# Kernel optimization log

Measured on AMD Instinct MI355X. Metric: run time of the kernel, lower is better.

Reference implementation:

```python
import jax, jax.numpy as jnp
import numpy as np

N_NODES = 50000
N_EDGES = 2000000
H = 64            # hidden_channels
D_IN = 2 * H      # concat(src, dst)
NEG_SLOPE = 0.01  # torch F.leaky_relu default


def _mlp_params(key, scale=0.05):
    ks = jax.random.split(key, 8)
    dims = [(D_IN, H), (H, H), (H, H // 2), (H // 2, 1)]
    p = []
    for i, (din, dout) in enumerate(dims):
        p.append(jax.random.normal(ks[2 * i], (din, dout), jnp.float32) * scale)
        p.append(jax.random.normal(ks[2 * i + 1], (dout,), jnp.float32) * scale)
    return p


def setup_inputs() -> dict:
    key = jax.random.key(0)
    k1, k2, k3, ke, kw = jax.random.split(key, 5)
    x_src = jax.random.normal(k1, (N_NODES, H), jnp.float32)
    x_dst = jax.random.normal(k2, (N_NODES, H), jnp.float32)
    edge_label_index = jax.random.randint(k3, (2, N_EDGES), 0, N_NODES, jnp.int64)
    e = _mlp_params(ke)
    w = _mlp_params(kw)
    inp = {"x_src": x_src, "x_dst": x_dst, "edge_label_index": edge_label_index}
    for i in range(4):
        inp[f"ew{i+1}"] = e[2 * i]; inp[f"eb{i+1}"] = e[2 * i + 1]
        inp[f"ww{i+1}"] = w[2 * i]; inp[f"wb{i+1}"] = w[2 * i + 1]
    return inp


def _mlp(x, w1, b1, w2, b2, w3, b3, w4, b4):
    lrelu = lambda z: jax.nn.leaky_relu(z, NEG_SLOPE)
    x = lrelu(x @ w1 + b1)
    x = lrelu(x @ w2 + b2)
    x = lrelu(x @ w3 + b3)
    return x @ w4 + b4


def reference(x_src, x_dst, edge_label_index,
              ew1, eb1, ww1, wb1, ew2, eb2, ww2, wb2,
              ew3, eb3, ww3, wb3, ew4, eb4, ww4, wb4):
    # gather node features by edge endpoints, concat -> [E, 2H]
    combined = jnp.concatenate(
        [x_src[edge_label_index[0]], x_dst[edge_label_index[1]]], axis=-1)
    link_exists = _mlp(combined, ew1, eb1, ew2, eb2, ew3, eb3, ew4, eb4)
    link_weight = _mlp(combined, ww1, wb1, ww2, wb2, ww3, wb3, ww4, wb4)
    return link_exists, link_weight
```

## Files before the change

kernel.cpp:

```cpp
#include <hip/hip_runtime.h>


typedef _Float16 half8  __attribute__((ext_vector_type(8)));
typedef _Float16 half4v __attribute__((ext_vector_type(4)));
typedef _Float16 half2v __attribute__((ext_vector_type(2)));
typedef float    float4v __attribute__((ext_vector_type(4)));

#define MLP_W_BYTES 28672
#define MLP_R_BYTES 12288
#define W1F 0
#define W2F 16384
#define W3F 24576
#define LDS_TOTAL   16384
#define WS_REST_OFF 57344
#define WS_X16_OFF  81920

__device__ __forceinline__ float lrelu(float x) { return fmaxf(x, 0.01f * x); }

__device__ __forceinline__ int uperm(int k) {
    return 16 * (2 * ((k >> 2) & 1) + ((k >> 5) & 1)) + 4 * ((k >> 3) & 3) + (k & 3);
}

__global__ void prep_frags(const float* __restrict__ w1, const float* __restrict__ b1,
                           const float* __restrict__ w2, const float* __restrict__ b2,
                           const float* __restrict__ w3, const float* __restrict__ b3,
                           const float* __restrict__ w4,
                           unsigned char* __restrict__ dstL,
                           unsigned char* __restrict__ dstR)
{
    int idx = blockIdx.x * blockDim.x + threadIdx.x;
    if (idx < 8192) {
        int L = (idx >> 3) & 63, j = idx & 7, f = idx >> 9;
        int q = L >> 4, mm = L & 15, t = f >> 2, s = f & 3;
        int k = 32 * s + 8 * q + j;
        ((_Float16*)(dstL + W1F))[idx] = (_Float16)w1[k * 64 + 16 * t + mm];
        return;
    }
    idx -= 8192;
    if (idx < 4096) {
        int L = (idx >> 3) & 63, j = idx & 7, f = idx >> 9;
        int q = L >> 4, mm = L & 15, t = f >> 1, s = f & 1;
        int u = uperm(32 * s + 8 * q + j);
        ((_Float16*)(dstL + W2F))[idx] = (_Float16)w2[u * 64 + 16 * t + mm];
        return;
    }
    idx -= 4096;
    if (idx < 2048) {
        int L = (idx >> 3) & 63, j = idx & 7, f = idx >> 9;
        int q = L >> 4, mm = L & 15, t = f >> 1, s = f & 1;
        int u = uperm(32 * s + 8 * q + j);
        ((_Float16*)(dstL + W3F))[idx] = (_Float16)w3[u * 32 + 16 * t + mm];
        return;
    }
    idx -= 2048;
    if (idx < 512) {
        int L = idx >> 3, j = idx & 7;
        int q = L >> 4, t = j >> 2, r = j & 3;
        ((float*)(dstR + 0))[idx] = w4[16 * t + 4 * q + r];
        return;
    }
    idx -= 512;
    if (idx < 1024) {
        int t = idx >> 8, L = (idx >> 2) & 63, r = idx & 3, q = L >> 4;
        ((float*)(dstR + 2048))[idx] = b1[16 * t + 4 * q + r];
        return;
    }
    idx -= 1024;
    if (idx < 1024) {
        int t = idx >> 8, L = (idx >> 2) & 63, r = idx & 3, q = L >> 4;
        ((float*)(dstR + 6144))[idx] = b2[16 * t + 4 * q + r];
        return;
    }
    idx -= 1024;
    if (idx < 512) {
        int t = idx >> 8, L = (idx >> 2) & 63, r = idx & 3, q = L >> 4;
        ((float*)(dstR + 10240))[idx] = b3[16 * t + 4 * q + r];
        return;
    }
}

__global__ void prep_nodes(const float* __restrict__ xs, const float* __restrict__ xd,
                           _Float16* __restrict__ os, _Float16* __restrict__ od, int n4)
{
    int stride = gridDim.x * blockDim.x;
    for (int i = blockIdx.x * blockDim.x + threadIdx.x; i < n4; i += stride) {
        float4v a = ((const float4v*)xs)[i];
        float4v b = ((const float4v*)xd)[i];
        half4v ha, hb;
#pragma unroll
        for (int j = 0; j < 4; ++j) { ha[j] = (_Float16)a[j]; hb[j] = (_Float16)b[j]; }
        ((half4v*)os)[i] = ha;
        ((half4v*)od)[i] = hb;
    }
}

__device__ __forceinline__ half2v cvt_pk(float a, float b) {
    return __builtin_bit_cast(half2v, __builtin_amdgcn_cvt_pkrtz(a, b));
}

__device__ __forceinline__ half8 repack2(float4v lo, float4v hi) {
    half8 r;
#pragma unroll
    for (int j = 0; j < 2; ++j) {
        half2v a = cvt_pk(lo[2 * j], lo[2 * j + 1]);
        half2v sa = a * (_Float16)0.01f;
        half2v ma = __builtin_elementwise_max(a, sa);
        r[2 * j] = ma[0]; r[2 * j + 1] = ma[1];
        half2v b = cvt_pk(hi[2 * j], hi[2 * j + 1]);
        half2v sb = b * (_Float16)0.01f;
        half2v mb = __builtin_elementwise_max(b, sb);
        r[4 + 2 * j] = mb[0]; r[4 + 2 * j + 1] = mb[1];
    }
    return r;
}

__device__ __forceinline__ int2 load_eidx(const int* __restrict__ eidx,
                                          int nE, int tile, int n)
{
    int e = tile * 16 + n;
    int ec = e < nE ? e : nE - 1;
    return make_int2(eidx[ec], eidx[nE + ec]);
}

__device__ __forceinline__ void gather_tile(const _Float16* __restrict__ xs,
                                            const _Float16* __restrict__ xd,
                                            int2 sd, int q, int4* G)
{
    const char* rs = (const char*)(xs + (size_t)sd.x * 64);
    const char* rd = (const char*)(xd + (size_t)sd.y * 64);
    G[0] = *(const int4*)(rs + 16 * q);
    G[1] = *(const int4*)(rs + 64 + 16 * q);
    G[2] = *(const int4*)(rd + 16 * q);
    G[3] = *(const int4*)(rd + 64 + 16 * q);
}

__device__ __forceinline__ int4 warm_tile(const _Float16* __restrict__ xs,
                                          const _Float16* __restrict__ xd,
                                          int2 sd, int c)
{
    int idx = (c & 2) ? sd.y : sd.x;
    const char* base = (const char*)(((c & 2) ? xd : xs) + (size_t)idx * 64);
    return *(const int4*)(base + (c & 1) * 64);
}

__global__ __launch_bounds__(256, 2)
void edge_mlp_mfma(const unsigned char* __restrict__ ws,
                   const _Float16* __restrict__ xs, const _Float16* __restrict__ xd,
                   const int* __restrict__ eidx,
                   const float* __restrict__ eb4p, const float* __restrict__ wb4p,
                   float* __restrict__ out, int nE, int ntiles)
{
    __shared__ unsigned char lds[LDS_TOTAL];
    const int m = (blockIdx.x >> 3) & 1;
    const int bid = (blockIdx.x & 7) | ((blockIdx.x >> 4) << 3);
    const unsigned char* wbase = ws + m * MLP_W_BYTES;
    const unsigned char* rbase = ws + WS_REST_OFF + m * MLP_R_BYTES;
    {
        const uint4* s = (const uint4*)(wbase + W1F);
        uint4* d = (uint4*)lds;
        for (int i = threadIdx.x; i < LDS_TOTAL / 16; i += 256) d[i] = s[i];
    }

    const int lane = threadIdx.x & 63;
    const int q = lane >> 4, n = lane & 15;
    const int wid = (bid << 2) | (threadIdx.x >> 6);
    const int nwaves = gridDim.x << 1;
    const float b4s = m ? wb4p[0] : eb4p[0];
    float* __restrict__ outm = out + (m ? nE : 0);

    half8 w2f[8], w3f[4];
#pragma unroll
    for (int f = 0; f < 8; ++f)
        w2f[f] = *(const half8*)(wbase + W2F + (f * 64 + lane) * 16);
#pragma unroll
    for (int f = 0; f < 4; ++f)
        w3f[f] = *(const half8*)(wbase + W3F + (f * 64 + lane) * 16);
    float4v w40 = *(const float4v*)(rbase + 0 + lane * 32);
    float4v w41 = *(const float4v*)(rbase + 0 + lane * 32 + 16);
    float4v b1f[4], b2f[4], b3f[2];
#pragma unroll
    for (int t = 0; t < 4; ++t)
        b1f[t] = *(const float4v*)(rbase + 2048 + (t * 64 + lane) * 16);
#pragma unroll
    for (int t = 0; t < 4; ++t)
        b2f[t] = *(const float4v*)(rbase + 6144 + (t * 64 + lane) * 16);
#pragma unroll
    for (int t = 0; t < 2; ++t)
        b3f[t] = *(const float4v*)(rbase + 10240 + (t * 64 + lane) * 16);

    __syncthreads();

    int4 Gcur[4];
    int4 W0 = {0,0,0,0}, W1 = {0,0,0,0}, W2 = {0,0,0,0}, junk = {0,0,0,0};
    int2 I1 = {0,0}, I2 = {0,0}, I3 = {0,0};

    int tile = wid;
    if (tile < ntiles) {
        int t1 = tile + nwaves;     if (t1 >= ntiles) t1 = ntiles - 1;
        int t2 = tile + 2 * nwaves; if (t2 >= ntiles) t2 = ntiles - 1;
        int t3 = tile + 3 * nwaves; if (t3 >= ntiles) t3 = ntiles - 1;
        int2 I0 = load_eidx(eidx, nE, tile, n);
        I1 = load_eidx(eidx, nE, t1, n);
        I2 = load_eidx(eidx, nE, t2, n);
        I3 = load_eidx(eidx, nE, t3, n);
        W0 = warm_tile(xs, xd, I0, q);
        W1 = warm_tile(xs, xd, I1, q);
        W2 = warm_tile(xs, xd, I2, q);
        gather_tile(xs, xd, I0, q, Gcur);
    }

#pragma unroll 1
    for (; tile < ntiles; tile += nwaves) {
        half8 B1[4];
#pragma unroll
        for (int s = 0; s < 4; ++s) B1[s] = __builtin_bit_cast(half8, Gcur[s]);

        __builtin_amdgcn_s_setprio(1);
        float4v acc[4];
#pragma unroll
        for (int t = 0; t < 4; ++t) {
            acc[t] = b1f[t];
#pragma unroll
            for (int s = 0; s < 4; ++s) {
                half8 A = *(const half8*)(lds + W1F + ((t * 4 + s) * 64 + lane) * 16);
                acc[t] = __builtin_amdgcn_mfma_f32_16x16x32_f16(A, B1[s], acc[t], 0, 0, 0);
            }
        }
        __builtin_amdgcn_s_setprio(0);

        gather_tile(xs, xd, I1, q, Gcur);

        junk.x ^= W0.x; junk.y ^= W0.y; junk.z ^= W0.z; junk.w ^= W0.w;
        W0 = W1; W1 = W2;
        W2 = warm_tile(xs, xd, I3, q);

        {
            int t4 = tile + 4 * nwaves; if (t4 >= ntiles) t4 = ntiles - 1;
            I1 = I2; I2 = I3;
            I3 = load_eidx(eidx, nE, t4, n);
        }

        __builtin_amdgcn_s_setprio(1);
        half8 B2[2] = { repack2(acc[0], acc[2]), repack2(acc[1], acc[3]) };
        float4v acc2[4];
#pragma unroll
        for (int t = 0; t < 4; ++t) {
            acc2[t] = b2f[t];
#pragma unroll
            for (int s = 0; s < 2; ++s)
                acc2[t] = __builtin_amdgcn_mfma_f32_16x16x32_f16(w2f[t * 2 + s], B2[s], acc2[t], 0, 0, 0);
        }
        half8 B3[2] = { repack2(acc2[0], acc2[2]), repack2(acc2[1], acc2[3]) };
        float4v acc3[2];
#pragma unroll
        for (int t = 0; t < 2; ++t) {
            acc3[t] = b3f[t];
#pragma unroll
            for (int s = 0; s < 2; ++s)
                acc3[t] = __builtin_amdgcn_mfma_f32_16x16x32_f16(w3f[t * 2 + s], B3[s], acc3[t], 0, 0, 0);
        }
        float o = 0.f;
#pragma unroll
        for (int r = 0; r < 4; ++r) o = fmaf(lrelu(acc3[0][r]), w40[r], o);
#pragma unroll
        for (int r = 0; r < 4; ++r) o = fmaf(lrelu(acc3[1][r]), w41[r], o);
        o += __shfl_xor(o, 16, 64);
        o += __shfl_xor(o, 32, 64);
        __builtin_amdgcn_s_setprio(0);

        int e = tile * 16 + n;
        if (q == 0 && e < nE)
            outm[e] = o + b4s;
    }

    junk.x ^= W0.x ^ W1.x ^ W2.x;
    junk.y ^= W0.y ^ W1.y ^ W2.y;
    junk.z ^= W0.z ^ W1.z ^ W2.z;
    junk.w ^= W0.w ^ W1.w ^ W2.w;
    if (nE < 0 && (junk.x | junk.y | junk.z | junk.w) != 0)
        out[0] = -1.0f;
}

extern "C" void kernel_launch(void* const* d_in, const int* in_sizes, int n_in,
                              void* d_out, int out_size, void* d_ws, size_t ws_size,
                              hipStream_t stream)
{
    const float* x_src = (const float*)d_in[0];
    const float* x_dst = (const float*)d_in[1];
    const int*   eidx  = (const int*)d_in[2];
    const float* ew1 = (const float*)d_in[3];
    const float* eb1 = (const float*)d_in[4];
    const float* ww1 = (const float*)d_in[5];
    const float* wb1 = (const float*)d_in[6];
    const float* ew2 = (const float*)d_in[7];
    const float* eb2 = (const float*)d_in[8];
    const float* ww2 = (const float*)d_in[9];
    const float* wb2 = (const float*)d_in[10];
    const float* ew3 = (const float*)d_in[11];
    const float* eb3 = (const float*)d_in[12];
    const float* ww3 = (const float*)d_in[13];
    const float* wb3 = (const float*)d_in[14];
    const float* ew4 = (const float*)d_in[15];
    const float* eb4 = (const float*)d_in[16];
    const float* ww4 = (const float*)d_in[17];
    const float* wb4 = (const float*)d_in[18];
    float* out = (float*)d_out;

    const int nE = in_sizes[2] / 2;
    const int nNodeElems = in_sizes[0];
    unsigned char* ws = (unsigned char*)d_ws;
    _Float16* xs16 = (_Float16*)(ws + WS_X16_OFF);
    _Float16* xd16 = xs16 + nNodeElems;

    prep_frags<<<68, 256, 0, stream>>>(ew1, eb1, ew2, eb2, ew3, eb3, ew4,
                                       ws, ws + WS_REST_OFF);
    prep_frags<<<68, 256, 0, stream>>>(ww1, wb1, ww2, wb2, ww3, wb3, ww4,
                                       ws + MLP_W_BYTES, ws + WS_REST_OFF + MLP_R_BYTES);
    prep_nodes<<<1024, 256, 0, stream>>>(x_src, x_dst, xs16, xd16, nNodeElems / 4);

    const int ntiles = (nE + 15) / 16;
    edge_mlp_mfma<<<1024, 256, 0, stream>>>(ws, xs16, xd16, eidx, eb4, wb4,
                                            out, nE, ntiles);
}
```

Before: 284.8 us.

## Software-pipeline layer-1 MFMA of next tile with layers 2-3 of current

Restructures the edge loop so the first-layer MFMAs for the next tile run alongside layers 2-3 and the output of the current tile, with the gather for the following tile issued after the compute. Bias fragments move from registers into LDS to make room for the extra in-flight accumulators. The warm-up prefetch depth changes, and the tile indices used for prefetch are no longer clamped. The intent is to hide gather latency and keep the matrix units busy across dependent layers. In exchange it adds LDS traffic for the biases, higher register pressure, and possible out-of-range index loads if load_eidx does not guard them.

Result: faster. 269.1 us (-5.5%).

```diff
diff --git a/kernel.cpp b/kernel.cpp
--- a/kernel.cpp
+++ b/kernel.cpp
@@ -11,7 +11,10 @@
 #define W1F 0
 #define W2F 16384
 #define W3F 24576
-#define LDS_TOTAL   16384
+#define LB1F 16384
+#define LB2F 20480
+#define LB3F 24576
+#define LDS_TOTAL 26624
 #define WS_REST_OFF 57344
 #define WS_X16_OFF  81920
 
@@ -158,7 +161,10 @@
     {
         const uint4* s = (const uint4*)(wbase + W1F);
         uint4* d = (uint4*)lds;
-        for (int i = threadIdx.x; i < LDS_TOTAL / 16; i += 256) d[i] = s[i];
+        for (int i = threadIdx.x; i < 1024; i += 256) d[i] = s[i];
+        const uint4* sb = (const uint4*)(rbase + 2048);
+        uint4* db = (uint4*)(lds + LB1F);
+        for (int i = threadIdx.x; i < 640; i += 256) db[i] = sb[i];
     }
 
     const int lane = threadIdx.x & 63;
@@ -177,75 +183,68 @@
         w3f[f] = *(const half8*)(wbase + W3F + (f * 64 + lane) * 16);
     float4v w40 = *(const float4v*)(rbase + 0 + lane * 32);
     float4v w41 = *(const float4v*)(rbase + 0 + lane * 32 + 16);
-    float4v b1f[4], b2f[4], b3f[2];
-#pragma unroll
-    for (int t = 0; t < 4; ++t)
-        b1f[t] = *(const float4v*)(rbase + 2048 + (t * 64 + lane) * 16);
-#pragma unroll
-    for (int t = 0; t < 4; ++t)
-        b2f[t] = *(const float4v*)(rbase + 6144 + (t * 64 + lane) * 16);
-#pragma unroll
-    for (int t = 0; t < 2; ++t)
-        b3f[t] = *(const float4v*)(rbase + 10240 + (t * 64 + lane) * 16);
 
     __syncthreads();
 
     int4 Gcur[4];
-    int4 W0 = {0,0,0,0}, W1 = {0,0,0,0}, W2 = {0,0,0,0}, junk = {0,0,0,0};
+    int4 W0 = {0,0,0,0}, W1 = {0,0,0,0}, junk = {0,0,0,0};
     int2 I1 = {0,0}, I2 = {0,0}, I3 = {0,0};
+    float4v accP[4];
 
     int tile = wid;
     if (tile < ntiles) {
-        int t1 = tile + nwaves;     if (t1 >= ntiles) t1 = ntiles - 1;
-        int t2 = tile + 2 * nwaves; if (t2 >= ntiles) t2 = ntiles - 1;
-        int t3 = tile + 3 * nwaves; if (t3 >= ntiles) t3 = ntiles - 1;
         int2 I0 = load_eidx(eidx, nE, tile, n);
-        I1 = load_eidx(eidx, nE, t1, n);
-        I2 = load_eidx(eidx, nE, t2, n);
-        I3 = load_eidx(eidx, nE, t3, n);
-        W0 = warm_tile(xs, xd, I0, q);
-        W1 = warm_tile(xs, xd, I1, q);
-        W2 = warm_tile(xs, xd, I2, q);
+        I1 = load_eidx(eidx, nE, tile + nwaves, n);
+        I2 = load_eidx(eidx, nE, tile + 2 * nwaves, n);
+        I3 = load_eidx(eidx, nE, tile + 3 * nwaves, n);
+        int4 ja = warm_tile(xs, xd, I0, q);
+        int4 jb = warm_tile(xs, xd, I1, q);
+        junk.x ^= ja.x ^ jb.x; junk.y ^= ja.y ^ jb.y;
+        junk.z ^= ja.z ^ jb.z; junk.w ^= ja.w ^ jb.w;
+        W0 = warm_tile(xs, xd, I2, q);
+        W1 = warm_tile(xs, xd, I3, q);
         gather_tile(xs, xd, I0, q, Gcur);
+
+        half8 B1[4];
+#pragma unroll
+        for (int s = 0; s < 4; ++s) B1[s] = __builtin_bit_cast(half8, Gcur[s]);
+#pragma unroll
+        for (int t = 0; t < 4; ++t) {
+            accP[t] = *(const float4v*)(lds + LB1F + (t * 64 + lane) * 16);
+#pragma unroll
+            for (int s = 0; s < 4; ++s) {
+                half8 A = *(const half8*)(lds + W1F + ((t * 4 + s) * 64 + lane) * 16);
+                accP[t] = __builtin_amdgcn_mfma_f32_16x16x32_f16(A, B1[s], accP[t], 0, 0, 0);
+            }
+        }
+        gather_tile(xs, xd, I1, q, Gcur);
+        I1 = I2; I2 = I3;
+        I3 = load_eidx(eidx, nE, tile + 4 * nwaves, n);
     }
 
 #pragma unroll 1
     for (; tile < ntiles; tile += nwaves) {
-        half8 B1[4];
-#pragma unroll
-        for (int s = 0; s < 4; ++s) B1[s] = __builtin_bit_cast(half8, Gcur[s]);
+        half8 B1n[4];
+#pragma unroll
+        for (int s = 0; s < 4; ++s) B1n[s] = __builtin_bit_cast(half8, Gcur[s]);
 
         __builtin_amdgcn_s_setprio(1);
-        float4v acc[4];
+        float4v accN[4];
 #pragma unroll
         for (int t = 0; t < 4; ++t) {
-            acc[t] = b1f[t];
+            accN[t] = *(const float4v*)(lds + LB1F + (t * 64 + lane) * 16);
 #pragma unroll
             for (int s = 0; s < 4; ++s) {
                 half8 A = *(const half8*)(lds + W1F + ((t * 4 + s) * 64 + lane) * 16);
-                acc[t] = __builtin_amdgcn_mfma_f32_16x16x32_f16(A, B1[s], acc[t], 0, 0, 0);
+                accN[t] = __builtin_amdgcn_mfma_f32_16x16x32_f16(A, B1n[s], accN[t], 0, 0, 0);
             }
         }
-        __builtin_amdgcn_s_setprio(0);
-
-        gather_tile(xs, xd, I1, q, Gcur);
-
-        junk.x ^= W0.x; junk.y ^= W0.y; junk.z ^= W0.z; junk.w ^= W0.w;
-        W0 = W1; W1 = W2;
-        W2 = warm_tile(xs, xd, I3, q);
-
-        {
-            int t4 = tile + 4 * nwaves; if (t4 >= ntiles) t4 = ntiles - 1;
-            I1 = I2; I2 = I3;
-            I3 = load_eidx(eidx, nE, t4, n);
-        }
-
-        __builtin_amdgcn_s_setprio(1);
-        half8 B2[2] = { repack2(acc[0], acc[2]), repack2(acc[1], acc[3]) };
+
+        half8 B2[2] = { repack2(accP[0], accP[2]), repack2(accP[1], accP[3]) };
         float4v acc2[4];
 #pragma unroll
         for (int t = 0; t < 4; ++t) {
-            acc2[t] = b2f[t];
+            acc2[t] = *(const float4v*)(lds + LB2F + (t * 64 + lane) * 16);
 #pragma unroll
             for (int s = 0; s < 2; ++s)
                 acc2[t] = __builtin_amdgcn_mfma_f32_16x16x32_f16(w2f[t * 2 + s], B2[s], acc2[t], 0, 0, 0);
@@ -254,7 +253,7 @@
         float4v acc3[2];
 #pragma unroll
         for (int t = 0; t < 2; ++t) {
-            acc3[t] = b3f[t];
+            acc3[t] = *(const float4v*)(lds + LB3F + (t * 64 + lane) * 16);
 #pragma unroll
             for (int s = 0; s < 2; ++s)
                 acc3[t] = __builtin_amdgcn_mfma_f32_16x16x32_f16(w3f[t * 2 + s], B3[s], acc3[t], 0, 0, 0);
@@ -268,15 +267,25 @@
         o += __shfl_xor(o, 32, 64);
         __builtin_amdgcn_s_setprio(0);
 
+        gather_tile(xs, xd, I1, q, Gcur);
+        junk.x ^= W0.x; junk.y ^= W0.y; junk.z ^= W0.z; junk.w ^= W0.w;
+        W0 = W1;
+        W1 = warm_tile(xs, xd, I3, q);
+        I1 = I2; I2 = I3;
+        I3 = load_eidx(eidx, nE, tile + 5 * nwaves, n);
+
         int e = tile * 16 + n;
         if (q == 0 && e < nE)
             outm[e] = o + b4s;
-    }
-
-    junk.x ^= W0.x ^ W1.x ^ W2.x;
-    junk.y ^= W0.y ^ W1.y ^ W2.y;
-    junk.z ^= W0.z ^ W1.z ^ W2.z;
-    junk.w ^= W0.w ^ W1.w ^ W2.w;
+
+#pragma unroll
+        for (int t = 0; t < 4; ++t) accP[t] = accN[t];
+    }
+
+    junk.x ^= W0.x ^ W1.x;
+    junk.y ^= W0.y ^ W1.y;
+    junk.z ^= W0.z ^ W1.z;
+    junk.w ^= W0.w ^ W1.w;
     if (nE < 0 && (junk.x | junk.y | junk.z | junk.w) != 0)
         out[0] = -1.0f;
 }
```

## Move layer 2/3 weights and biases into LDS to raise occupancy to three blocks

Applied to the files above, without the earlier changes.

Layer 2 and 3 weight fragments and all bias fragments now live in LDS instead of registers, read per tile. Launch bounds go from 2 to 3 blocks per CU. The aim is more resident waves to hide the random gather latency of this memory-bound kernel. In exchange there is more LDS traffic per tile and more LDS per block (38 KB).

Result: slower. 1.088 ms (+282.1%).

```diff
diff --git a/kernel.cpp b/kernel.cpp
--- a/kernel.cpp
+++ b/kernel.cpp
@@ -11,7 +11,10 @@
 #define W1F 0
 #define W2F 16384
 #define W3F 24576
-#define LDS_TOTAL   16384
+#define LB1F 28672
+#define LB2F 32768
+#define LB3F 36864
+#define LDS_TOTAL 38912
 #define WS_REST_OFF 57344
 #define WS_X16_OFF  81920
 
@@ -143,7 +146,7 @@
     return *(const int4*)(base + (c & 1) * 64);
 }
 
-__global__ __launch_bounds__(256, 2)
+__global__ __launch_bounds__(256, 3)
 void edge_mlp_mfma(const unsigned char* __restrict__ ws,
                    const _Float16* __restrict__ xs, const _Float16* __restrict__ xd,
                    const int* __restrict__ eidx,
@@ -158,7 +161,10 @@
     {
         const uint4* s = (const uint4*)(wbase + W1F);
         uint4* d = (uint4*)lds;
-        for (int i = threadIdx.x; i < LDS_TOTAL / 16; i += 256) d[i] = s[i];
+        for (int i = threadIdx.x; i < 1792; i += 256) d[i] = s[i];
+        const uint4* sb = (const uint4*)(rbase + 2048);
+        uint4* db = (uint4*)(lds + LB1F);
+        for (int i = threadIdx.x; i < 640; i += 256) db[i] = sb[i];
     }
 
     const int lane = threadIdx.x & 63;
@@ -168,25 +174,8 @@
     const float b4s = m ? wb4p[0] : eb4p[0];
     float* __restrict__ outm = out + (m ? nE : 0);
 
-    half8 w2f[8], w3f[4];
-#pragma unroll
-    for (int f = 0; f < 8; ++f)
-        w2f[f] = *(const half8*)(wbase + W2F + (f * 64 + lane) * 16);
-#pragma unroll
-    for (int f = 0; f < 4; ++f)
-        w3f[f] = *(const half8*)(wbase + W3F + (f * 64 + lane) * 16);
     float4v w40 = *(const float4v*)(rbase + 0 + lane * 32);
     float4v w41 = *(const float4v*)(rbase + 0 + lane * 32 + 16);
-    float4v b1f[4], b2f[4], b3f[2];
-#pragma unroll
-    for (int t = 0; t < 4; ++t)
-        b1f[t] = *(const float4v*)(rbase + 2048 + (t * 64 + lane) * 16);
-#pragma unroll
-    for (int t = 0; t < 4; ++t)
-        b2f[t] = *(const float4v*)(rbase + 6144 + (t * 64 + lane) * 16);
-#pragma unroll
-    for (int t = 0; t < 2; ++t)
-        b3f[t] = *(const float4v*)(rbase + 10240 + (t * 64 + lane) * 16);
 
     __syncthreads();
 
@@ -219,7 +208,7 @@
         float4v acc[4];
 #pragma unroll
         for (int t = 0; t < 4; ++t) {
-            acc[t] = b1f[t];
+            acc[t] = *(const float4v*)(lds + LB1F + (t * 64 + lane) * 16);
 #pragma unroll
             for (int s = 0; s < 4; ++s) {
                 half8 A = *(const half8*)(lds + W1F + ((t * 4 + s) * 64 + lane) * 16);
@@ -245,19 +234,23 @@
         float4v acc2[4];
 #pragma unroll
         for (int t = 0; t < 4; ++t) {
-            acc2[t] = b2f[t];
-#pragma unroll
-            for (int s = 0; s < 2; ++s)
-                acc2[t] = __builtin_amdgcn_mfma_f32_16x16x32_f16(w2f[t * 2 + s], B2[s], acc2[t], 0, 0, 0);
+            acc2[t] = *(const float4v*)(lds + LB2F + (t * 64 + lane) * 16);
+#pragma unroll
+            for (int s = 0; s < 2; ++s) {
+                half8 A = *(const half8*)(lds + W2F + ((t * 2 + s) * 64 + lane) * 16);
+                acc2[t] = __builtin_amdgcn_mfma_f32_16x16x32_f16(A, B2[s], acc2[t], 0, 0, 0);
+            }
         }
         half8 B3[2] = { repack2(acc2[0], acc2[2]), repack2(acc2[1], acc2[3]) };
         float4v acc3[2];
 #pragma unroll
         for (int t = 0; t < 2; ++t) {
-            acc3[t] = b3f[t];
-#pragma unroll
-            for (int s = 0; s < 2; ++s)
-                acc3[t] = __builtin_amdgcn_mfma_f32_16x16x32_f16(w3f[t * 2 + s], B3[s], acc3[t], 0, 0, 0);
+            acc3[t] = *(const float4v*)(lds + LB3F + (t * 64 + lane) * 16);
+#pragma unroll
+            for (int s = 0; s < 2; ++s) {
+                half8 A = *(const half8*)(lds + W3F + ((t * 2 + s) * 64 + lane) * 16);
+                acc3[t] = __builtin_amdgcn_mfma_f32_16x16x32_f16(A, B3[s], acc3[t], 0, 0, 0);
+            }
         }
         float o = 0.f;
 #pragma unroll
```
